# Kernel tuning notes

Measured on AMD Instinct MI355X. Metric: run time of the kernel, lower is better.

## Reference

```python
import jax, jax.numpy as jnp
import numpy as np

N_ENT = 16384   # num_entities
N_REL = 50      # num relations
D = 128         # embedding dim
B = 4           # num bases
E = 262144      # num edges (avg degree 16)


def setup_inputs() -> dict:
    key = jax.random.key(0)
    k1, k2, k3, k4, k5, k6 = jax.random.split(key, 6)
    x = jax.random.normal(k1, (N_ENT, D), dtype=jnp.float32)
    bases = jax.random.normal(k2, (B, D, D), dtype=jnp.float32) * 0.05
    comps = jax.random.normal(k3, (N_REL, B), dtype=jnp.float32)
    alpha = jax.random.normal(k4, (N_REL, 1), dtype=jnp.float32)
    edge_index = jax.random.randint(k5, (2, E), 0, N_ENT, dtype=jnp.int64)
    edge_type = jax.random.randint(k6, (E,), 0, N_REL, dtype=jnp.int64)
    return {"x": x, "bases": bases, "comps": comps, "alpha": alpha,
            "edge_index": edge_index, "edge_type": edge_type}


def reference(x, bases, comps, alpha, edge_index, edge_type):
    # R-GCN basis-decomposition message passing:
    #   msg_e = (h_j @ W_{r(e)}) * alpha_{r(e)} * norm_e,  W_r = sum_b comps[r,b] * bases[b]
    #   out_i = sum_{e: row(e)=i} msg_e
    n = x.shape[0]
    row, col = edge_index[0], edge_index[1]

    # edge_norm = 1/sqrt(D_row) * 1/sqrt(D_col) with out-degree over rows
    ones = jnp.ones(row.shape, x.dtype)
    deg = jax.ops.segment_sum(ones, row, num_segments=n)
    deg_inv = jnp.where(deg > 0, jax.lax.rsqrt(jnp.maximum(deg, 1.0)), 0.0)
    norm = deg_inv[row] * deg_inv[col]               # [E]

    h_j = x[col]                                     # [E, D] gather
    c_e = comps[edge_type]                           # [E, B] gather
    # sum_b c[e,b] * (h_j[e] @ bases[b])  ==  einsum over (b,d)
    hj_b = c_e[:, :, None] * h_j[:, None, :]         # [E, B, D]
    msg = jnp.einsum('ebd,bdf->ef', hj_b, bases)     # [E, D] big GEMM
    msg = msg * alpha[edge_type] * norm[:, None]

    out = jax.ops.segment_sum(msg, row, num_segments=n)  # scatter-add to nodes
    return out
```

## Files before the change

kernel.cpp:

```cpp
#include <hip/hip_runtime.h>
#include <stdint.h>

#define NENT 16384
#define NREL 50
#define NE   262144
#define BSTR 64

typedef __attribute__((ext_vector_type(8))) short short8;
typedef __attribute__((ext_vector_type(4))) float float4v;

__device__ __forceinline__ uint32_t fpack(float a, float b){
  uint32_t ua = __float_as_uint(a), ub = __float_as_uint(b);
  ua = (ua + 0x7fffu + ((ua >> 16) & 1u)) >> 16;
  ub = (ub + 0x7fffu + ((ub >> 16) & 1u)) >> 16;
  return ua | (ub << 16);
}
__device__ __forceinline__ unsigned short f2bf(float a){
  uint32_t ua = __float_as_uint(a);
  return (unsigned short)((ua + 0x7fffu + ((ua >> 16) & 1u)) >> 16);
}
__device__ __forceinline__ float rdlane_f(float v, int j){
  return __uint_as_float((uint32_t)__builtin_amdgcn_readlane((int)__float_as_uint(v), j));
}

__global__ void k_prep0(int* __restrict__ deg,
                        const float* __restrict__ alpha, const float* __restrict__ comps,
                        float* __restrict__ acomb,
                        const float* __restrict__ W, unsigned short* __restrict__ WT){
  int gid = blockIdx.x * 256 + threadIdx.x;
  if (gid < NENT) deg[gid] = 0;
  if (gid < NREL * 4) acomb[gid] = alpha[gid >> 2] * comps[gid];
  int n = gid >> 9, k = gid & 511;
  WT[gid] = f2bf(W[k * 128 + n]);
}

__global__ void k_fill_bkt(const int* __restrict__ eidx, const int* __restrict__ etype,
                           int* __restrict__ deg, uint32_t* __restrict__ bucket){
  int e = blockIdx.x * 256 + threadIdx.x;
  int row = eidx[e], col = eidx[NE + e], r = etype[e];
  int pos = atomicAdd(&deg[row], 1);
  if (pos < BSTR) bucket[row * BSTR + pos] = (uint32_t)col | ((uint32_t)r << 14);
}

__global__ __launch_bounds__(256) void k_agg(
    const float* __restrict__ x, const int* __restrict__ deg,
    const float* __restrict__ acomb, const uint32_t* __restrict__ bucket,
    uint32_t* __restrict__ Au){
  int lane = threadIdx.x & 63;
  int i = (blockIdx.x * 256 + threadIdx.x) >> 6;
  int o = i * 256 + lane;
  int d = deg[i];
  if (d == 0){ Au[o] = 0; Au[o+64] = 0; Au[o+128] = 0; Au[o+192] = 0; return; }
  int de = min(d, BSTR);
  float di = rsqrtf((float)d);
  uint32_t rec = bucket[i * BSTR + min(lane, de - 1)];
  int  colL = (int)(rec & 0x3FFFu);
  int  rL   = (int)(rec >> 14);
  int  dc   = deg[colL];
  float wL  = (lane < de && dc > 0) ? di * rsqrtf((float)dc) : 0.f;
  float4 ac = ((const float4*)acomb)[rL];
  float w0 = wL * ac.x, w1 = wL * ac.y, w2 = wL * ac.z, w3 = wL * ac.w;
  const float2* xf2 = (const float2*)x;
  float a0=0,a1=0,a2=0,a3=0,a4=0,a5=0,a6=0,a7=0;
  int rde = (de + 3) & ~3;
  for (int j = 0; j < rde; j += 4){
    #pragma unroll
    for (int jj = 0; jj < 4; ++jj){
      int   cj = __builtin_amdgcn_readlane(colL, j + jj);
      float m0 = rdlane_f(w0, j + jj), m1 = rdlane_f(w1, j + jj);
      float m2 = rdlane_f(w2, j + jj), m3 = rdlane_f(w3, j + jj);
      float2 h = xf2[cj * 64 + lane];
      a0 += m0*h.x; a1 += m0*h.y;
      a2 += m1*h.x; a3 += m1*h.y;
      a4 += m2*h.x; a5 += m2*h.y;
      a6 += m3*h.x; a7 += m3*h.y;
    }
  }
  Au[o]       = fpack(a0, a1);
  Au[o + 64]  = fpack(a2, a3);
  Au[o + 128] = fpack(a4, a5);
  Au[o + 192] = fpack(a6, a7);
}

__global__ __launch_bounds__(256) void k_gemm(
    const uint32_t* __restrict__ Au, const unsigned short* __restrict__ WT,
    float* __restrict__ outf){
  int lane = threadIdx.x & 63;
  int wv   = threadIdx.x >> 6;
  int m16  = lane & 15;
  int quad = lane >> 4;
  int m0   = blockIdx.x * 16;
  const short8* Arow = (const short8*)(Au + (m0 + m16) * 256);
  int c0 = (wv * 2) * 16 + m16, c1 = (wv * 2 + 1) * 16 + m16;
  const short8* B0 = (const short8*)(WT + c0 * 512);
  const short8* B1 = (const short8*)(WT + c1 * 512);
  float4v acc0 = {0.f,0.f,0.f,0.f}, acc1 = {0.f,0.f,0.f,0.f};
  #pragma unroll
  for (int k0 = 0; k0 < 512; k0 += 32){
    int idx = (k0 >> 3) + quad;
    short8 aF = Arow[idx];
    acc0 = __builtin_amdgcn_mfma_f32_16x16x32_bf16(aF, B0[idx], acc0, 0, 0, 0);
    acc1 = __builtin_amdgcn_mfma_f32_16x16x32_bf16(aF, B1[idx], acc1, 0, 0, 0);
  }
  int mrow = m0 + quad * 4;
  #pragma unroll
  for (int r = 0; r < 4; ++r){
    outf[(mrow + r) * 128 + c0] = acc0[r];
    outf[(mrow + r) * 128 + c1] = acc1[r];
  }
}

extern "C" void kernel_launch(void* const* d_in, const int* in_sizes, int n_in,
                              void* d_out, int out_size, void* d_ws, size_t ws_size,
                              hipStream_t stream){
  (void)in_sizes; (void)n_in; (void)out_size; (void)ws_size;
  const float* x     = (const float*)d_in[0];
  const float* bases = (const float*)d_in[1];
  const float* comps = (const float*)d_in[2];
  const float* alpha = (const float*)d_in[3];
  const int* eidx    = (const int*)d_in[4];
  const int* etype   = (const int*)d_in[5];
  char* ws = (char*)d_ws;

  int*      deg    = (int*)      (ws + 0);
  float*    acomb  = (float*)    (ws + (64  << 10));
  unsigned short* WT = (unsigned short*)(ws + (128 << 10));
  uint32_t* bucket = (uint32_t*) (ws + (512 << 10));
  uint32_t* Au     = (uint32_t*) (ws + (5u  << 20));

  k_prep0   <<<256, 256, 0, stream>>>(deg, alpha, comps, acomb, bases, WT);
  k_fill_bkt<<<NE / 256, 256, 0, stream>>>(eidx, etype, deg, bucket);
  k_agg     <<<NENT / 4, 256, 0, stream>>>(x, deg, acomb, bucket, Au);
  k_gemm    <<<NENT / 16, 256, 0, stream>>>(Au, WT, (float*)d_out);
}
```

Measured before the change: 127.0 us.

## Fuse aggregation and GEMM via LDS and gather bf16 node features

Merges the per-node aggregation kernel and the MFMA GEMM into one kernel: each block aggregates 16 rows into a padded LDS tile, then runs the bf16 MFMA GEMM from LDS. This removes the intermediate Au global buffer round trip and one launch. The prep kernel also converts x to packed bf16 so the edge gathers read half the bytes. The trade-off is that each block now processes only 16 rows, four per wave, serially, which may cost aggregation parallelism, and rounding features to bf16 before aggregation adds precision loss.

New measurement: 119.7 us. -5.7%, faster.

```diff
diff --git a/kernel.cpp b/kernel.cpp
--- a/kernel.cpp
+++ b/kernel.cpp
@@ -5,10 +5,12 @@
 #define NREL 50
 #define NE   262144
 #define BSTR 64
+#define ASTR 260
 
 typedef __attribute__((ext_vector_type(8))) short short8;
 typedef __attribute__((ext_vector_type(4))) float float4v;
 
+__device__ __forceinline__ float bf2f(uint32_t u){ return __uint_as_float(u << 16); }
 __device__ __forceinline__ uint32_t fpack(float a, float b){
   uint32_t ua = __float_as_uint(a), ub = __float_as_uint(b);
   ua = (ua + 0x7fffu + ((ua >> 16) & 1u)) >> 16;
@@ -26,12 +28,25 @@
 __global__ void k_prep0(int* __restrict__ deg,
                         const float* __restrict__ alpha, const float* __restrict__ comps,
                         float* __restrict__ acomb,
-                        const float* __restrict__ W, unsigned short* __restrict__ WT){
+                        const float* __restrict__ W, unsigned short* __restrict__ WT,
+                        const float* __restrict__ x, uint32_t* __restrict__ xbf){
   int gid = blockIdx.x * 256 + threadIdx.x;
   if (gid < NENT) deg[gid] = 0;
   if (gid < NREL * 4) acomb[gid] = alpha[gid >> 2] * comps[gid];
-  int n = gid >> 9, k = gid & 511;
-  WT[gid] = f2bf(W[k * 128 + n]);
+  {
+    int n = gid >> 9, k = gid & 511;
+    WT[gid] = f2bf(W[k * 128 + n]);
+  }
+  {
+    const float4* xin = (const float4*)(x + gid * 32);
+    uint32_t* xo = xbf + gid * 16;
+    #pragma unroll
+    for (int j = 0; j < 8; ++j){
+      float4 p = xin[j];
+      xo[j * 2]     = fpack(p.x, p.y);
+      xo[j * 2 + 1] = fpack(p.z, p.w);
+    }
+  }
 }
 
 __global__ void k_fill_bkt(const int* __restrict__ eidx, const int* __restrict__ etype,
@@ -42,67 +57,69 @@
   if (pos < BSTR) bucket[row * BSTR + pos] = (uint32_t)col | ((uint32_t)r << 14);
 }
 
-__global__ __launch_bounds__(256) void k_agg(
-    const float* __restrict__ x, const int* __restrict__ deg,
+__global__ __launch_bounds__(256) void k_fused(
+    const uint32_t* __restrict__ xbf, const int* __restrict__ deg,
     const float* __restrict__ acomb, const uint32_t* __restrict__ bucket,
-    uint32_t* __restrict__ Au){
-  int lane = threadIdx.x & 63;
-  int i = (blockIdx.x * 256 + threadIdx.x) >> 6;
-  int o = i * 256 + lane;
-  int d = deg[i];
-  if (d == 0){ Au[o] = 0; Au[o+64] = 0; Au[o+128] = 0; Au[o+192] = 0; return; }
-  int de = min(d, BSTR);
-  float di = rsqrtf((float)d);
-  uint32_t rec = bucket[i * BSTR + min(lane, de - 1)];
-  int  colL = (int)(rec & 0x3FFFu);
-  int  rL   = (int)(rec >> 14);
-  int  dc   = deg[colL];
-  float wL  = (lane < de && dc > 0) ? di * rsqrtf((float)dc) : 0.f;
-  float4 ac = ((const float4*)acomb)[rL];
-  float w0 = wL * ac.x, w1 = wL * ac.y, w2 = wL * ac.z, w3 = wL * ac.w;
-  const float2* xf2 = (const float2*)x;
-  float a0=0,a1=0,a2=0,a3=0,a4=0,a5=0,a6=0,a7=0;
-  int rde = (de + 3) & ~3;
-  for (int j = 0; j < rde; j += 4){
-    #pragma unroll
-    for (int jj = 0; jj < 4; ++jj){
-      int   cj = __builtin_amdgcn_readlane(colL, j + jj);
-      float m0 = rdlane_f(w0, j + jj), m1 = rdlane_f(w1, j + jj);
-      float m2 = rdlane_f(w2, j + jj), m3 = rdlane_f(w3, j + jj);
-      float2 h = xf2[cj * 64 + lane];
-      a0 += m0*h.x; a1 += m0*h.y;
-      a2 += m1*h.x; a3 += m1*h.y;
-      a4 += m2*h.x; a5 += m2*h.y;
-      a6 += m3*h.x; a7 += m3*h.y;
+    const unsigned short* __restrict__ WT, float* __restrict__ outf)
+{
+  __shared__ uint32_t A_lds[16 * ASTR];
+  int t = threadIdx.x, lane = t & 63, wv = t >> 6;
+  int row0 = blockIdx.x * 16;
+
+  for (int rr = wv * 4; rr < wv * 4 + 4; ++rr){
+    int i = row0 + rr;
+    int d = deg[i];
+    uint32_t* Arow = &A_lds[rr * ASTR];
+    if (d == 0){
+      Arow[lane] = 0; Arow[lane+64] = 0; Arow[lane+128] = 0; Arow[lane+192] = 0;
+      continue;
     }
+    int de = min(d, BSTR);
+    float di = rsqrtf((float)d);
+    uint32_t rec = bucket[i * BSTR + min(lane, de - 1)];
+    int colL = (int)(rec & 0x3FFFu);
+    int rL   = (int)(rec >> 14);
+    int dc   = deg[colL];
+    float wL = (lane < de && dc > 0) ? di * rsqrtf((float)dc) : 0.f;
+    float4 ac = ((const float4*)acomb)[rL];
+    float w0 = wL*ac.x, w1 = wL*ac.y, w2 = wL*ac.z, w3 = wL*ac.w;
+    float a0=0,a1=0,a2=0,a3=0,a4=0,a5=0,a6=0,a7=0;
+    int rde = (de + 3) & ~3;
+    for (int j = 0; j < rde; j += 4){
+      #pragma unroll
+      for (int jj = 0; jj < 4; ++jj){
+        int   cj = __builtin_amdgcn_readlane(colL, j + jj);
+        float m0 = rdlane_f(w0, j + jj), m1 = rdlane_f(w1, j + jj);
+        float m2 = rdlane_f(w2, j + jj), m3 = rdlane_f(w3, j + jj);
+        uint32_t hv = xbf[cj * 64 + lane];
+        float h0 = bf2f(hv & 0xffffu), h1 = bf2f(hv >> 16);
+        a0 += m0*h0; a1 += m0*h1;
+        a2 += m1*h0; a3 += m1*h1;
+        a4 += m2*h0; a5 += m2*h1;
+        a6 += m3*h0; a7 += m3*h1;
+      }
+    }
+    Arow[lane]       = fpack(a0, a1);
+    Arow[lane + 64]  = fpack(a2, a3);
+    Arow[lane + 128] = fpack(a4, a5);
+    Arow[lane + 192] = fpack(a6, a7);
   }
-  Au[o]       = fpack(a0, a1);
-  Au[o + 64]  = fpack(a2, a3);
-  Au[o + 128] = fpack(a4, a5);
-  Au[o + 192] = fpack(a6, a7);
-}
+  __syncthreads();
 
-__global__ __launch_bounds__(256) void k_gemm(
-    const uint32_t* __restrict__ Au, const unsigned short* __restrict__ WT,
-    float* __restrict__ outf){
-  int lane = threadIdx.x & 63;
-  int wv   = threadIdx.x >> 6;
-  int m16  = lane & 15;
-  int quad = lane >> 4;
-  int m0   = blockIdx.x * 16;
-  const short8* Arow = (const short8*)(Au + (m0 + m16) * 256);
-  int c0 = (wv * 2) * 16 + m16, c1 = (wv * 2 + 1) * 16 + m16;
+  int m16 = lane & 15, quad = lane >> 4;
+  int c0 = (wv * 2) * 16 + m16, c1 = c0 + 16;
   const short8* B0 = (const short8*)(WT + c0 * 512);
   const short8* B1 = (const short8*)(WT + c1 * 512);
+  const uint32_t* Abase = &A_lds[m16 * ASTR];
   float4v acc0 = {0.f,0.f,0.f,0.f}, acc1 = {0.f,0.f,0.f,0.f};
   #pragma unroll
   for (int k0 = 0; k0 < 512; k0 += 32){
+    short8 aF = *(const short8*)&Abase[(k0 >> 1) + quad * 4];
     int idx = (k0 >> 3) + quad;
-    short8 aF = Arow[idx];
     acc0 = __builtin_amdgcn_mfma_f32_16x16x32_bf16(aF, B0[idx], acc0, 0, 0, 0);
     acc1 = __builtin_amdgcn_mfma_f32_16x16x32_bf16(aF, B1[idx], acc1, 0, 0, 0);
   }
-  int mrow = m0 + quad * 4;
+  int mrow = row0 + quad * 4;
   #pragma unroll
   for (int r = 0; r < 4; ++r){
     outf[(mrow + r) * 128 + c0] = acc0[r];
@@ -125,11 +142,10 @@
   int*      deg    = (int*)      (ws + 0);
   float*    acomb  = (float*)    (ws + (64  << 10));
   unsigned short* WT = (unsigned short*)(ws + (128 << 10));
-  uint32_t* bucket = (uint32_t*) (ws + (512 << 10));
-  uint32_t* Au     = (uint32_t*) (ws + (5u  << 20));
+  uint32_t* xbf    = (uint32_t*) (ws + (512 << 10));
+  uint32_t* bucket = (uint32_t*) (ws + (5u  << 20));
 
-  k_prep0   <<<256, 256, 0, stream>>>(deg, alpha, comps, acomb, bases, WT);
+  k_prep0   <<<256, 256, 0, stream>>>(deg, alpha, comps, acomb, bases, WT, x, xbf);
   k_fill_bkt<<<NE / 256, 256, 0, stream>>>(eidx, etype, deg, bucket);
-  k_agg     <<<NENT / 4, 256, 0, stream>>>(x, deg, acomb, bucket, Au);
-  k_gemm    <<<NENT / 16, 256, 0, stream>>>(Au, WT, (float*)d_out);
+  k_fused   <<<NENT / 16, 256, 0, stream>>>(xbf, deg, acomb, bucket, WT, (float*)d_out);
 }
```
